# Optimization experiments

Measured on AMD Instinct MI355X. Metric: run time of the kernel, lower is better.

Reference implementation:

```python
import jax, jax.numpy as jnp
import numpy as np
from jax import lax

# IntraVoxelVolterra (reconstructed semantics of the MVC CUDA ext):
#   log_forward(x, w)  = 3D 'same' conv of log(x) with kernel w [O,k,k,k,I]
#                        (log-domain conv: log(prod_window x^w))
#   exp_forward(v, x)  = x * exp(v)  (multiplicative Volterra update of the field)
#   forward(x) = x * exp(conv(log x, w1) + conv(log x, w2) * conv(log x, w3))

B, CI, CO, K, D = 2, 32, 32, 3, 64
W_SCALE = 0.005  # keep exp() numerically sane given 27*32 accumulated log terms


def _conv_log(xl, w):
    # xl: [B, CI, D, H, W]; w: [CO, k, k, k, CI] -> [B, CO, D, H, W]
    return lax.conv_general_dilated(
        xl, w, window_strides=(1, 1, 1), padding='SAME',
        dimension_numbers=('NCDHW', 'ODHWI', 'NCDHW'))


def setup_inputs() -> dict:
    key = jax.random.key(0)
    k0, k1, k2, k3 = jax.random.split(key, 4)
    # x must be strictly positive (log-domain); fODF amplitudes are nonnegative
    x = jax.random.uniform(k0, (B, CI, D, D, D), dtype=jnp.float32,
                           minval=0.05, maxval=1.0)
    wshape = (CO, K, K, K, CI)
    w1 = jax.random.uniform(k1, wshape, dtype=jnp.float32) * W_SCALE
    w2 = jax.random.uniform(k2, wshape, dtype=jnp.float32) * W_SCALE
    w3 = jax.random.uniform(k3, wshape, dtype=jnp.float32) * W_SCALE
    return {"x": x, "w1": w1, "w2": w2, "w3": w3}


def reference(x, w1, w2, w3):
    xl = jnp.log(x)                      # [B, CI, D, H, W]
    log1 = _conv_log(xl, w1)             # [B, CO, D, H, W]
    log2 = _conv_log(xl, w2)
    log3 = _conv_log(xl, w3)
    # Volterra combination in log domain, then multiplicative exp update
    return x * jnp.exp(log1 + log2 * log3)
```

## Files before the change

### kernel.cpp

```cpp
#include <hip/hip_runtime.h>

typedef unsigned short u16;
typedef unsigned int   u32;
typedef __attribute__((ext_vector_type(8)))  short bf16x8;
typedef __attribute__((ext_vector_type(4)))  float f32x4;
typedef __attribute__((ext_vector_type(4)))  u32   u32x4;

#define BB   2
#define NCH  32
#define DD   64
#define PD   66
#define NTAP 27
#define D3   (DD * DD * DD)

#define NROW 18
#define XCHK 68
#define RS   (XCHK * 8)
#define QS   (NROW * RS + 8)

__device__ __forceinline__ u16 f2bf(float f) {
  u32 u = __float_as_uint(f);
  u = (u + 0x7fffu + ((u >> 16) & 1u)) >> 16;
  return (u16)u;
}

__device__ __forceinline__ void glds16(const u16* g, u16* l) {
  __builtin_amdgcn_global_load_lds(
      (const __attribute__((address_space(1))) u32*)(const void*)g,
      (__attribute__((address_space(3))) u32*)(void*)l, 16, 0, 0);
}

__global__ void pack_w_kernel(const float* __restrict__ w1,
                              const float* __restrict__ w2,
                              const float* __restrict__ w3,
                              u16* __restrict__ wb) {
  int i = blockIdx.x * 256 + threadIdx.x;
  if (i >= NTAP * 3 * 2 * 512) return;
  int j    = i & 7;
  int lane = (i >> 3) & 63;
  int nh   = (i >> 9) & 1;
  int q    = i >> 10;
  int c    = q % 3;
  int tap  = q / 3;
  int o  = nh * 16 + (lane & 15);
  int ci = (lane >> 4) * 8 + j;
  const float* ws = (c == 0) ? w1 : (c == 1) ? w2 : w3;
  wb[i] = f2bf(ws[(size_t)o * (NTAP * NCH) + tap * NCH + ci]);
}

__global__ void zero_halo_kernel(u16* __restrict__ xl) {
  int tid = blockIdx.x * 256 + threadIdx.x;
  if (tid >= BB * PD * PD * PD) return;
  int xp = tid % PD;
  int t  = tid / PD;
  int yp = t % PD;  t /= PD;
  int zp = t % PD;
  if (xp && yp && zp && xp < PD - 1 && yp < PD - 1 && zp < PD - 1) return;
  u32x4 z4 = {0u, 0u, 0u, 0u};
  u32x4* dst = (u32x4*)(xl + (size_t)tid * NCH);
#pragma unroll
  for (int i = 0; i < 4; i++) dst[i] = z4;
}

__global__ __launch_bounds__(256) void build_xl_kernel(const float* __restrict__ x,
                                                       u16* __restrict__ xl) {
  __shared__ __align__(16) u16 lds[256][40];
  int bi = blockIdx.x;
  int yt = bi & 15;
  int z  = (bi >> 4) & 63;
  int b  = bi >> 10;
  int t  = threadIdx.x;
  int x4 = t & 15, yy = (t >> 4) & 3, c0 = t >> 6;
  int y0 = yt * 4;

  const float* src = x + (size_t)b * NCH * D3 + ((size_t)z * DD + (y0 + yy)) * DD + x4 * 4;
  int v0 = yy * 64 + x4 * 4;
#pragma unroll
  for (int p = 0; p < 8; p++) {
    int c = c0 + 4 * p;
    f32x4 f = *(const f32x4*)(src + (size_t)c * D3);
#pragma unroll
    for (int k = 0; k < 4; k++) lds[v0 + k][c] = f2bf(__logf(f[k]));
  }
  __syncthreads();

  int vy = t >> 6, vx = t & 63;
  u16* dst = xl + ((((size_t)b * PD + (z + 1)) * PD + (y0 + vy + 1)) * PD + (vx + 1)) * NCH;
#pragma unroll
  for (int q = 0; q < 4; q++)
    *(bf16x8*)(dst + q * 8) = *(const bf16x8*)&lds[t][q * 8];
}

__global__ __launch_bounds__(256, 2) void conv_volterra_kernel(
    const u16* __restrict__ xl, const u16* __restrict__ wb,
    const float* __restrict__ x, float* __restrict__ out) {
  __shared__ __align__(16) u16 tile[4 * QS];

  int i = blockIdx.x;
  int xcd = i & 7, r = i >> 3;
  int z  = xcd * 8 + (r >> 5);
  int yt = (r >> 1) & 15;
  int b  = r & 1;
  int y0 = yt * 4;

  int tid = threadIdx.x, wv = tid >> 6, lane = tid & 63;
  int l15 = lane & 15, l4 = lane >> 4;
  int p = wv >> 1, nh = wv & 1;

  const u16* gbase = xl + (((size_t)b * PD + z) * PD + y0) * PD * NCH;

  {
    u16* ldsq = tile + wv * QS;
#pragma unroll
    for (int rr = 0; rr < NROW; ++rr) {
      const int zs = rr / 6, yr = rr % 6;
      glds16(gbase + ((size_t)(zs * PD + yr)) * PD * NCH + lane * NCH + wv * 8,
             ldsq + rr * RS);
    }
  }
  if (tid < 144) {
    int q = tid & 3, u = tid >> 2;
    int rr = u >> 1, xt = 64 + (u & 1);
    int zs = rr / 6, yr = rr - zs * 6;
    const u16* g = gbase + ((size_t)(zs * PD + yr)) * PD * NCH + xt * NCH + q * 8;
    u32x4 v = *(const u32x4*)g;
    *(u32x4*)(tile + q * QS + rr * RS + xt * 8) = v;
  }
  __syncthreads();

  f32x4 acc[3][8];
#pragma unroll
  for (int c = 0; c < 3; c++)
#pragma unroll
    for (int m = 0; m < 8; m++)
      acc[c][m] = (f32x4){0.f, 0.f, 0.f, 0.f};

  const u16* A0 = tile + (size_t)l4 * QS + (size_t)(2 * p) * RS + (size_t)l15 * 8;
  const u16* wB = wb + nh * 512 + lane * 8;

#pragma unroll
  for (int kd = 0; kd < 3; ++kd)
#pragma unroll
    for (int khy = 0; khy < 3; ++khy)
#pragma unroll
      for (int kw = 0; kw < 3; ++kw) {
        const int tap = (kd * 3 + khy) * 3 + kw;
        bf16x8 bwf[3];
#pragma unroll
        for (int c = 0; c < 3; c++)
          bwf[c] = *(const bf16x8*)(wB + (size_t)(tap * 3 + c) * 1024);
        bf16x8 a[8];
#pragma unroll
        for (int m = 0; m < 8; m++)
          a[m] = *(const bf16x8*)(A0 + (kd * 6 + (m >> 2) + khy) * RS
                                     + ((m & 3) * 16 + kw) * 8);
#pragma unroll
        for (int m = 0; m < 8; m++)
#pragma unroll
          for (int c = 0; c < 3; c++)
            acc[c][m] = __builtin_amdgcn_mfma_f32_16x16x32_bf16(
                a[m], bwf[c], acc[c][m], 0, 0, 0);
      }

  const int o = nh * 16 + l15;
  const int ybase = y0 + 2 * p;
  const size_t pb = (size_t)(b * NCH + o) * D3 + (size_t)z * DD * DD;
#pragma unroll
  for (int m = 0; m < 8; m++) {
    int y  = ybase + (m >> 2);
    int xc = (m & 3) * 16 + l4 * 4;
    size_t idx = pb + (size_t)y * DD + xc;
    f32x4 xv = *(const f32x4*)(x + idx);
    f32x4 rr;
#pragma unroll
    for (int j = 0; j < 4; j++)
      rr[j] = xv[j] * __expf(acc[0][m][j] + acc[1][m][j] * acc[2][m][j]);
    *(f32x4*)(out + idx) = rr;
  }
}

extern "C" void kernel_launch(void* const* d_in, const int* in_sizes, int n_in,
                              void* d_out, int out_size, void* d_ws, size_t ws_size,
                              hipStream_t stream) {
  const float* x  = (const float*)d_in[0];
  const float* w1 = (const float*)d_in[1];
  const float* w2 = (const float*)d_in[2];
  const float* w3 = (const float*)d_in[3];
  float* out = (float*)d_out;
  u16* xl = (u16*)d_ws;
  u16* wb = xl + (size_t)BB * PD * PD * PD * NCH;

  pack_w_kernel<<<(NTAP * 3 * 2 * 512 + 255) / 256, 256, 0, stream>>>(w1, w2, w3, wb);
  const int npad = BB * PD * PD * PD;
  zero_halo_kernel<<<(npad + 255) / 256, 256, 0, stream>>>(xl);
  build_xl_kernel<<<BB * DD * 16, 256, 0, stream>>>(x, xl);
  conv_volterra_kernel<<<2048, 256, 0, stream>>>(xl, wb, x, out);
}
```

Measured before the change: 188.2 us.

## Stream z-planes through LDS ring buffer with prefetch across 8 depths per block

```diff
diff --git a/kernel.cpp b/kernel.cpp
--- a/kernel.cpp
+++ b/kernel.cpp
@@ -13,10 +13,9 @@
 #define NTAP 27
 #define D3   (DD * DD * DD)
 
-#define NROW 18
-#define XCHK 68
-#define RS   (XCHK * 8)
-#define QS   (NROW * RS + 8)
+#define RS   (66 * 8)
+#define QSS  (6 * RS)
+#define PS   (4 * QSS)
 
 __device__ __forceinline__ u16 f2bf(float f) {
   u32 u = __float_as_uint(f);
@@ -91,92 +90,99 @@
     *(bf16x8*)(dst + q * 8) = *(const bf16x8*)&lds[t][q * 8];
 }
 
-__global__ __launch_bounds__(256, 2) void conv_volterra_kernel(
+__global__ __launch_bounds__(512, 2) void conv_volterra_kernel(
     const u16* __restrict__ xl, const u16* __restrict__ wb,
     const float* __restrict__ x, float* __restrict__ out) {
-  __shared__ __align__(16) u16 tile[4 * QS];
+  __shared__ __align__(16) u16 tile[4 * PS];
 
   int i = blockIdx.x;
-  int xcd = i & 7, r = i >> 3;
-  int z  = xcd * 8 + (r >> 5);
-  int yt = (r >> 1) & 15;
-  int b  = r & 1;
+  int zc = i & 7, r = i >> 3;
+  int yt = r & 15;
+  int b  = r >> 4;
   int y0 = yt * 4;
+  int z0 = zc * 8;
 
   int tid = threadIdx.x, wv = tid >> 6, lane = tid & 63;
   int l15 = lane & 15, l4 = lane >> 4;
-  int p = wv >> 1, nh = wv & 1;
-
-  const u16* gbase = xl + (((size_t)b * PD + z) * PD + y0) * PD * NCH;
-
-  {
-    u16* ldsq = tile + wv * QS;
-#pragma unroll
-    for (int rr = 0; rr < NROW; ++rr) {
-      const int zs = rr / 6, yr = rr % 6;
-      glds16(gbase + ((size_t)(zs * PD + yr)) * PD * NCH + lane * NCH + wv * 8,
-             ldsq + rr * RS);
+  int yy = wv >> 1, nh = wv & 1;
+
+  const u16* wB = wb + nh * 512 + lane * 8;
+  const u16* xlb = xl + (size_t)b * PD * PD * PD * NCH;
+
+#define STAGE(P)                                                               \
+  {                                                                            \
+    const int p_ = (P);                                                        \
+    u16* dst_ = tile + (p_ & 3) * PS + (wv >> 1) * QSS + ((wv & 1) * 3) * RS;  \
+    const u16* src_ = xlb + (((size_t)p_ * PD) + (y0 + (wv & 1) * 3)) * PD * NCH \
+                    + lane * NCH + (wv >> 1) * 8;                              \
+    _Pragma("unroll")                                                          \
+    for (int k_ = 0; k_ < 3; k_++)                                             \
+      glds16(src_ + (size_t)k_ * PD * NCH, dst_ + k_ * RS);                    \
+    if (tid < 48) {                                                            \
+      int q_ = tid & 3, u_ = tid >> 2;                                         \
+      int row_ = u_ >> 1, xt_ = 64 + (u_ & 1);                                 \
+      u32x4 v_ = *(const u32x4*)(xlb + (((size_t)p_ * PD) + (y0 + row_)) * PD * NCH \
+                                 + xt_ * NCH + q_ * 8);                        \
+      *(u32x4*)(tile + (p_ & 3) * PS + q_ * QSS + row_ * RS + xt_ * 8) = v_;   \
+    }                                                                          \
+  }
+
+  STAGE(z0); STAGE(z0 + 1); STAGE(z0 + 2);
+  __syncthreads();
+
+#pragma unroll 1
+  for (int zi = 0; zi < 8; ++zi) {
+    const int z = z0 + zi;
+    if (zi < 7) STAGE(z + 3);
+
+    f32x4 acc[3][4];
+#pragma unroll
+    for (int c = 0; c < 3; c++)
+#pragma unroll
+      for (int m = 0; m < 4; m++) acc[c][m] = (f32x4){0.f, 0.f, 0.f, 0.f};
+
+#pragma unroll
+    for (int kd = 0; kd < 3; ++kd) {
+      const u16* Ap = tile + ((z + kd) & 3) * PS + l4 * QSS;
+#pragma unroll
+      for (int khy = 0; khy < 3; ++khy) {
+        const u16* Ar = Ap + (yy + khy) * RS + l15 * 8;
+#pragma unroll
+        for (int kw = 0; kw < 3; ++kw) {
+          const int tap = (kd * 3 + khy) * 3 + kw;
+          bf16x8 bwf[3];
+#pragma unroll
+          for (int c = 0; c < 3; c++)
+            bwf[c] = *(const bf16x8*)(wB + (size_t)(tap * 3 + c) * 1024);
+          bf16x8 a[4];
+#pragma unroll
+          for (int m = 0; m < 4; m++)
+            a[m] = *(const bf16x8*)(Ar + (m * 16 + kw) * 8);
+#pragma unroll
+          for (int m = 0; m < 4; m++)
+#pragma unroll
+            for (int c = 0; c < 3; c++)
+              acc[c][m] = __builtin_amdgcn_mfma_f32_16x16x32_bf16(
+                  a[m], bwf[c], acc[c][m], 0, 0, 0);
+        }
+      }
     }
+
+    const int o = nh * 16 + l15;
+    const size_t pb = (size_t)(b * NCH + o) * D3 + ((size_t)z * DD + (y0 + yy)) * DD;
+#pragma unroll
+    for (int m = 0; m < 4; m++) {
+      size_t idx = pb + m * 16 + l4 * 4;
+      f32x4 xv = *(const f32x4*)(x + idx);
+      f32x4 rr;
+#pragma unroll
+      for (int j = 0; j < 4; j++)
+        rr[j] = xv[j] * __expf(acc[0][m][j] + acc[1][m][j] * acc[2][m][j]);
+      *(f32x4*)(out + idx) = rr;
+    }
+    __syncthreads();
   }
-  if (tid < 144) {
-    int q = tid & 3, u = tid >> 2;
-    int rr = u >> 1, xt = 64 + (u & 1);
-    int zs = rr / 6, yr = rr - zs * 6;
-    const u16* g = gbase + ((size_t)(zs * PD + yr)) * PD * NCH + xt * NCH + q * 8;
-    u32x4 v = *(const u32x4*)g;
-    *(u32x4*)(tile + q * QS + rr * RS + xt * 8) = v;
-  }
-  __syncthreads();
-
-  f32x4 acc[3][8];
-#pragma unroll
-  for (int c = 0; c < 3; c++)
-#pragma unroll
-    for (int m = 0; m < 8; m++)
-      acc[c][m] = (f32x4){0.f, 0.f, 0.f, 0.f};
-
-  const u16* A0 = tile + (size_t)l4 * QS + (size_t)(2 * p) * RS + (size_t)l15 * 8;
-  const u16* wB = wb + nh * 512 + lane * 8;
-
-#pragma unroll
-  for (int kd = 0; kd < 3; ++kd)
-#pragma unroll
-    for (int khy = 0; khy < 3; ++khy)
-#pragma unroll
-      for (int kw = 0; kw < 3; ++kw) {
-        const int tap = (kd * 3 + khy) * 3 + kw;
-        bf16x8 bwf[3];
-#pragma unroll
-        for (int c = 0; c < 3; c++)
-          bwf[c] = *(const bf16x8*)(wB + (size_t)(tap * 3 + c) * 1024);
-        bf16x8 a[8];
-#pragma unroll
-        for (int m = 0; m < 8; m++)
-          a[m] = *(const bf16x8*)(A0 + (kd * 6 + (m >> 2) + khy) * RS
-                                     + ((m & 3) * 16 + kw) * 8);
-#pragma unroll
-        for (int m = 0; m < 8; m++)
-#pragma unroll
-          for (int c = 0; c < 3; c++)
-            acc[c][m] = __builtin_amdgcn_mfma_f32_16x16x32_bf16(
-                a[m], bwf[c], acc[c][m], 0, 0, 0);
-      }
-
-  const int o = nh * 16 + l15;
-  const int ybase = y0 + 2 * p;
-  const size_t pb = (size_t)(b * NCH + o) * D3 + (size_t)z * DD * DD;
-#pragma unroll
-  for (int m = 0; m < 8; m++) {
-    int y  = ybase + (m >> 2);
-    int xc = (m & 3) * 16 + l4 * 4;
-    size_t idx = pb + (size_t)y * DD + xc;
-    f32x4 xv = *(const f32x4*)(x + idx);
-    f32x4 rr;
-#pragma unroll
-    for (int j = 0; j < 4; j++)
-      rr[j] = xv[j] * __expf(acc[0][m][j] + acc[1][m][j] * acc[2][m][j]);
-    *(f32x4*)(out + idx) = rr;
-  }
+#undef STAGE
 }
 
 extern "C" void kernel_launch(void* const* d_in, const int* in_sizes, int n_in,
@@ -194,5 +200,5 @@
   const int npad = BB * PD * PD * PD;
   zero_halo_kernel<<<(npad + 255) / 256, 256, 0, stream>>>(xl);
   build_xl_kernel<<<BB * DD * 16, 256, 0, stream>>>(x, xl);
-  conv_volterra_kernel<<<2048, 256, 0, stream>>>(xl, wb, x, out);
-}
+  conv_volterra_kernel<<<256, 512, 0, stream>>>(xl, wb, x, out);
+}
```

Result: slower. 275.0 us (+46.1%).

## Split log-input into channel-quarter planes and double conv block to 512 threads

Applied to the files above, without the earlier changes.

```diff
diff --git a/kernel.cpp b/kernel.cpp
--- a/kernel.cpp
+++ b/kernel.cpp
@@ -2,6 +2,7 @@
 
 typedef unsigned short u16;
 typedef unsigned int   u32;
+typedef unsigned long long u64;
 typedef __attribute__((ext_vector_type(8)))  short bf16x8;
 typedef __attribute__((ext_vector_type(4)))  float f32x4;
 typedef __attribute__((ext_vector_type(4)))  u32   u32x4;
@@ -13,10 +14,12 @@
 #define NTAP 27
 #define D3   (DD * DD * DD)
 
-#define NROW 18
-#define XCHK 68
-#define RS   (XCHK * 8)
-#define QS   (NROW * RS + 8)
+#define PLANE ((size_t)BB * PD * PD * PD * 8)
+#define XOFF(b, zp, yp, xp) \
+  (((((size_t)(b) * PD + (zp)) * PD + (yp)) * PD + (xp)) * 8)
+
+#define RS   (68 * 8)
+#define QS   (18 * RS + 8)
 
 __device__ __forceinline__ u16 f2bf(float f) {
   u32 u = __float_as_uint(f);
@@ -48,23 +51,25 @@
   wb[i] = f2bf(ws[(size_t)o * (NTAP * NCH) + tap * NCH + ci]);
 }
 
-__global__ void zero_halo_kernel(u16* __restrict__ xl) {
+__global__ void zero_halo_kernel(u16* __restrict__ xlq) {
   int tid = blockIdx.x * 256 + threadIdx.x;
   if (tid >= BB * PD * PD * PD) return;
   int xp = tid % PD;
   int t  = tid / PD;
   int yp = t % PD;  t /= PD;
   int zp = t % PD;
+  int b  = t / PD;
   if (xp && yp && zp && xp < PD - 1 && yp < PD - 1 && zp < PD - 1) return;
   u32x4 z4 = {0u, 0u, 0u, 0u};
-  u32x4* dst = (u32x4*)(xl + (size_t)tid * NCH);
-#pragma unroll
-  for (int i = 0; i < 4; i++) dst[i] = z4;
+  size_t off = XOFF(b, zp, yp, xp);
+#pragma unroll
+  for (int q = 0; q < 4; q++)
+    *(u32x4*)(xlq + q * PLANE + off) = z4;
 }
 
 __global__ __launch_bounds__(256) void build_xl_kernel(const float* __restrict__ x,
-                                                       u16* __restrict__ xl) {
-  __shared__ __align__(16) u16 lds[256][40];
+                                                       u16* __restrict__ xlq) {
+  __shared__ u64 ldsT[32][66];
   int bi = blockIdx.x;
   int yt = bi & 15;
   int z  = (bi >> 4) & 63;
@@ -74,25 +79,35 @@
   int y0 = yt * 4;
 
   const float* src = x + (size_t)b * NCH * D3 + ((size_t)z * DD + (y0 + yy)) * DD + x4 * 4;
-  int v0 = yy * 64 + x4 * 4;
+  int i0 = yy * 16 + x4;
 #pragma unroll
   for (int p = 0; p < 8; p++) {
     int c = c0 + 4 * p;
     f32x4 f = *(const f32x4*)(src + (size_t)c * D3);
-#pragma unroll
-    for (int k = 0; k < 4; k++) lds[v0 + k][c] = f2bf(__logf(f[k]));
+    u64 pk = (u64)f2bf(__logf(f[0]))
+           | ((u64)f2bf(__logf(f[1])) << 16)
+           | ((u64)f2bf(__logf(f[2])) << 32)
+           | ((u64)f2bf(__logf(f[3])) << 48);
+    ldsT[c][i0] = pk;
   }
   __syncthreads();
 
-  int vy = t >> 6, vx = t & 63;
-  u16* dst = xl + ((((size_t)b * PD + (z + 1)) * PD + (y0 + vy + 1)) * PD + (vx + 1)) * NCH;
-#pragma unroll
-  for (int q = 0; q < 4; q++)
-    *(bf16x8*)(dst + q * 8) = *(const bf16x8*)&lds[t][q * 8];
-}
-
-__global__ __launch_bounds__(256, 2) void conv_volterra_kernel(
-    const u16* __restrict__ xl, const u16* __restrict__ wb,
+  int q = t >> 6, lv = t & 63;
+  const u16* ldsu = (const u16*)ldsT;
+#pragma unroll
+  for (int m = 0; m < 4; m++) {
+    int v = m * 64 + lv;
+    int iw = v >> 2, hs = v & 3;
+    bf16x8 val;
+#pragma unroll
+    for (int j = 0; j < 8; j++)
+      val[j] = (short)ldsu[((q * 8 + j) * 66 + iw) * 4 + hs];
+    *(bf16x8*)(xlq + q * PLANE + XOFF(b, z + 1, y0 + m + 1, lv + 1)) = val;
+  }
+}
+
+__global__ __launch_bounds__(512, 4) void conv_volterra_kernel(
+    const u16* __restrict__ xlq, const u16* __restrict__ wb,
     const float* __restrict__ x, float* __restrict__ out) {
   __shared__ __align__(16) u16 tile[4 * QS];
 
@@ -105,43 +120,42 @@
 
   int tid = threadIdx.x, wv = tid >> 6, lane = tid & 63;
   int l15 = lane & 15, l4 = lane >> 4;
-  int p = wv >> 1, nh = wv & 1;
-
-  const u16* gbase = xl + (((size_t)b * PD + z) * PD + y0) * PD * NCH;
+  int yy = wv >> 1, nh = wv & 1;
 
   {
-    u16* ldsq = tile + wv * QS;
-#pragma unroll
-    for (int rr = 0; rr < NROW; ++rr) {
-      const int zs = rr / 6, yr = rr % 6;
-      glds16(gbase + ((size_t)(zs * PD + yr)) * PD * NCH + lane * NCH + wv * 8,
-             ldsq + rr * RS);
+    int sq = wv & 3, h = wv >> 2;
+    const u16* gq = xlq + sq * PLANE;
+    u16* ldsq = tile + sq * QS;
+#pragma unroll
+    for (int k = 0; k < 9; k++) {
+      const int zs = k / 3, yrb = 2 * (k % 3);
+      glds16(gq + XOFF(b, z + zs, y0 + yrb + h, 0) + lane * 8,
+             ldsq + ((zs * 6 + yrb + h) * RS));
     }
   }
   if (tid < 144) {
     int q = tid & 3, u = tid >> 2;
     int rr = u >> 1, xt = 64 + (u & 1);
     int zs = rr / 6, yr = rr - zs * 6;
-    const u16* g = gbase + ((size_t)(zs * PD + yr)) * PD * NCH + xt * NCH + q * 8;
-    u32x4 v = *(const u32x4*)g;
+    u32x4 v = *(const u32x4*)(xlq + q * PLANE + XOFF(b, z + zs, y0 + yr, xt));
     *(u32x4*)(tile + q * QS + rr * RS + xt * 8) = v;
   }
   __syncthreads();
 
-  f32x4 acc[3][8];
+  f32x4 acc[3][4];
 #pragma unroll
   for (int c = 0; c < 3; c++)
 #pragma unroll
-    for (int m = 0; m < 8; m++)
-      acc[c][m] = (f32x4){0.f, 0.f, 0.f, 0.f};
-
-  const u16* A0 = tile + (size_t)l4 * QS + (size_t)(2 * p) * RS + (size_t)l15 * 8;
+    for (int m = 0; m < 4; m++) acc[c][m] = (f32x4){0.f, 0.f, 0.f, 0.f};
+
+  const u16* A0 = tile + (size_t)l4 * QS + (size_t)l15 * 8;
   const u16* wB = wb + nh * 512 + lane * 8;
 
 #pragma unroll
   for (int kd = 0; kd < 3; ++kd)
 #pragma unroll
-    for (int khy = 0; khy < 3; ++khy)
+    for (int khy = 0; khy < 3; ++khy) {
+      const u16* Ar = A0 + (kd * 6 + yy + khy) * RS;
 #pragma unroll
       for (int kw = 0; kw < 3; ++kw) {
         const int tap = (kd * 3 + khy) * 3 + kw;
@@ -149,27 +163,24 @@
 #pragma unroll
         for (int c = 0; c < 3; c++)
           bwf[c] = *(const bf16x8*)(wB + (size_t)(tap * 3 + c) * 1024);
-        bf16x8 a[8];
-#pragma unroll
-        for (int m = 0; m < 8; m++)
-          a[m] = *(const bf16x8*)(A0 + (kd * 6 + (m >> 2) + khy) * RS
-                                     + ((m & 3) * 16 + kw) * 8);
-#pragma unroll
-        for (int m = 0; m < 8; m++)
+        bf16x8 a[4];
+#pragma unroll
+        for (int m = 0; m < 4; m++)
+          a[m] = *(const bf16x8*)(Ar + (m * 16 + kw) * 8);
+#pragma unroll
+        for (int m = 0; m < 4; m++)
 #pragma unroll
           for (int c = 0; c < 3; c++)
             acc[c][m] = __builtin_amdgcn_mfma_f32_16x16x32_bf16(
                 a[m], bwf[c], acc[c][m], 0, 0, 0);
       }
+    }
 
   const int o = nh * 16 + l15;
-  const int ybase = y0 + 2 * p;
-  const size_t pb = (size_t)(b * NCH + o) * D3 + (size_t)z * DD * DD;
-#pragma unroll
-  for (int m = 0; m < 8; m++) {
-    int y  = ybase + (m >> 2);
-    int xc = (m & 3) * 16 + l4 * 4;
-    size_t idx = pb + (size_t)y * DD + xc;
+  const size_t pb = (size_t)(b * NCH + o) * D3 + ((size_t)z * DD + (y0 + yy)) * DD;
+#pragma unroll
+  for (int m = 0; m < 4; m++) {
+    size_t idx = pb + m * 16 + l4 * 4;
     f32x4 xv = *(const f32x4*)(x + idx);
     f32x4 rr;
 #pragma unroll
@@ -187,12 +198,12 @@
   const float* w2 = (const float*)d_in[2];
   const float* w3 = (const float*)d_in[3];
   float* out = (float*)d_out;
-  u16* xl = (u16*)d_ws;
-  u16* wb = xl + (size_t)BB * PD * PD * PD * NCH;
+  u16* xlq = (u16*)d_ws;
+  u16* wb  = xlq + 4 * PLANE;
 
   pack_w_kernel<<<(NTAP * 3 * 2 * 512 + 255) / 256, 256, 0, stream>>>(w1, w2, w3, wb);
   const int npad = BB * PD * PD * PD;
-  zero_halo_kernel<<<(npad + 255) / 256, 256, 0, stream>>>(xl);
-  build_xl_kernel<<<BB * DD * 16, 256, 0, stream>>>(x, xl);
-  conv_volterra_kernel<<<2048, 256, 0, stream>>>(xl, wb, x, out);
-}
+  zero_halo_kernel<<<(npad + 255) / 256, 256, 0, stream>>>(xlq);
+  build_xl_kernel<<<BB * DD * 16, 256, 0, stream>>>(x, xlq);
+  conv_volterra_kernel<<<2048, 512, 0, stream>>>(xlq, wb, x, out);
+}
```

After: 193.0 us. 1.03x slower.
